# Optimization experiments

Measured on AMD Instinct MI355X. Metric: run time of the kernel, lower is better.

The kernel has to match this reference:

```python
import jax, jax.numpy as jnp
import numpy as np

MIN_NORM = 1e-7

def _norm(x):
    return jnp.maximum(jnp.sqrt(jnp.sum(x * x, axis=-1, keepdims=True)), MIN_NORM)

def _artanh(x):
    return jnp.arctanh(jnp.clip(x, -1.0 + 1e-6, 1.0 - 1e-6))

def tan_k(x, k):
    sq = jnp.sqrt(-k)
    return jnp.tanh(sq * x) / sq

def artan_k(x, k):
    sq = jnp.sqrt(-k)
    return _artanh(sq * x) / sq

def mobius_add(x, y, k):
    xy = jnp.sum(x * y, axis=-1, keepdims=True)
    x2 = jnp.sum(x * x, axis=-1, keepdims=True)
    y2 = jnp.sum(y * y, axis=-1, keepdims=True)
    num = (1.0 - 2.0 * k * xy - k * y2) * x + (1.0 + k * x2) * y
    den = 1.0 - 2.0 * k * xy + (k * k) * x2 * y2
    return num / jnp.maximum(den, MIN_NORM)

def expmap0(u, k):
    un = _norm(u)
    return tan_k(un, k) * u / un

def logmap0(y, k):
    yn = _norm(y)
    return artan_k(yn, k) * y / yn

def mobius_matvec(M, x, k):
    mx = x @ M.T
    xn = _norm(x)
    mxn = _norm(mx)
    return tan_k(mxn / xn * artan_k(xn, k), k) * mx / mxn

def mobius_pmul(w, x, k):
    wx = w * x
    xn = _norm(x)
    wxn = _norm(wx)
    return tan_k(wxn / xn * artan_k(xn, k), k) * wx / wxn

def setup_inputs() -> dict:
    B, S, D_IN, H = 64, 128, 768, 768
    key = jax.random.key(0)
    ks = jax.random.split(key, 5)
    stdv = 1.0 / np.sqrt(H)
    # inputs scaled small so points lie well inside the Poincare ball
    inputs = jax.random.normal(ks[0], (B, S, D_IN), dtype=jnp.float32) * 1e-3
    timestamps = jax.random.uniform(ks[1], (B, S), dtype=jnp.float32)
    h0 = jnp.zeros((B, H), dtype=jnp.float32)
    c0 = jnp.zeros((B, H), dtype=jnp.float32)
    W_all = jax.random.uniform(ks[2], (H, 4 * H), minval=-stdv, maxval=stdv, dtype=jnp.float32)
    U_all = jax.random.uniform(ks[3], (4 * H, D_IN), minval=-stdv, maxval=stdv, dtype=jnp.float32)
    W_d = jax.random.uniform(ks[4], (H, H), minval=-stdv, maxval=stdv, dtype=jnp.float32)
    c = jnp.float32(-1.0)  # Poincare ball curvature
    return {"inputs": inputs, "timestamps": timestamps, "h0": h0, "c0": c0,
            "W_all": W_all, "U_all": U_all, "W_d": W_d, "c": c}

def reference(inputs, timestamps, h0, c0, W_all, U_all, W_d, c):
    k = c
    W_f, W_i, W_o, W_ct = jnp.split(W_all, 4, axis=1)
    U_f, U_i, U_o, U_ct = jnp.split(U_all, 4, axis=0)

    def one_rnn_transform(W, h, U, x):
        return mobius_add(mobius_matvec(W, h, k), mobius_matvec(U, x, k), k)

    def step(carry, xs):
        h, cc = carry
        x, t = xs  # x: (B, D_in), t: (B,)
        c_s1 = expmap0(jnp.tanh(logmap0(mobius_matvec(W_d, cc, k), k)), k)
        t_exp = jnp.broadcast_to(t[:, None], c_s1.shape)
        c_s2 = mobius_pmul(c_s1, t_exp, k)
        c_l = mobius_add(-c_s1, cc, k)
        c_adj = mobius_add(c_l, c_s2, k)
        f = jax.nn.sigmoid(logmap0(one_rnn_transform(W_f, h, U_f, x), k))
        i = jax.nn.sigmoid(logmap0(one_rnn_transform(W_i, h, U_i, x), k))
        o = jax.nn.sigmoid(logmap0(one_rnn_transform(W_o, h, U_o, x), k))
        c_tmp = jax.nn.sigmoid(logmap0(one_rnn_transform(W_ct, h, U_ct, x), k))
        new_c = mobius_add(mobius_pmul(i, c_tmp, k), mobius_pmul(f, c_adj, k), k)
        new_h = mobius_pmul(o, expmap0(jnp.tanh(new_c), k), k)
        return (new_h, new_c), o

    xs = (inputs.transpose(1, 0, 2), timestamps.T)  # seq-major for scan
    (h_last, c_last), outs = jax.lax.scan(step, (h0, c0), xs)
    outputs = outs.transpose(1, 0, 2)  # (B, S, H)
    return (outputs, h_last, c_last)
```

## Files before the change

kernel.cpp:

```cpp
#include <hip/hip_runtime.h>
#include <hip/hip_bf16.h>
#include <math.h>

#define MINN 1e-7f

#define BB 64
#define SS 128
#define NCOL 3840

typedef float f4 __attribute__((ext_vector_type(4)));
typedef short bf16x8 __attribute__((ext_vector_type(8)));
typedef float f32x4 __attribute__((ext_vector_type(4)));

__device__ __forceinline__ float artanh_c(float x) {
  x = fminf(fmaxf(x, -1.0f + 1e-6f), 1.0f - 1e-6f);
  return atanhf(x);
}
__device__ __forceinline__ float tan_k_(float x, float sq) { return tanhf(sq * x) / sq; }
__device__ __forceinline__ float artan_k_(float x, float sq) { return artanh_c(sq * x) / sq; }

template <int N>
__device__ __forceinline__ void block_reduce_sum(float* v, float* red) {
#pragma unroll
  for (int m = 1; m < 64; m <<= 1) {
#pragma unroll
    for (int i = 0; i < N; ++i) v[i] += __shfl_xor(v[i], m, 64);
  }
  int wid = threadIdx.x >> 6;
  int lane = threadIdx.x & 63;
  if (lane == 0) {
#pragma unroll
    for (int i = 0; i < N; ++i) red[wid * N + i] = v[i];
  }
  __syncthreads();
#pragma unroll
  for (int i = 0; i < N; ++i) v[i] = red[i] + red[N + i] + red[2 * N + i] + red[3 * N + i];
  __syncthreads();
}

__global__ __launch_bounds__(256) void k_build_cw(const float* __restrict__ W_all,
                                                  const float* __restrict__ W_d,
                                                  __hip_bfloat16* __restrict__ CWh,
                                                  __hip_bfloat16* __restrict__ CWl) {
  int col = blockIdx.x;
#pragma unroll
  for (int p = 0; p < 3; ++p) {
    int k = threadIdx.x + 256 * p;
    float v;
    if (col < 768) {
      v = W_d[col * 768 + k];
    } else {
      int jm = col - 768;
      int g = jm / 768;
      int j2 = jm - g * 768;
      v = W_all[j2 * 3072 + g * 768 + k];
    }
    __hip_bfloat16 h = __float2bfloat16(v);
    CWh[(size_t)col * 768 + k] = h;
    CWl[(size_t)col * 768 + k] = __float2bfloat16(v - __bfloat162float(h));
  }
}

__global__ __launch_bounds__(256) void k_init_state(
    const float* __restrict__ h0, const float* __restrict__ c0,
    float* __restrict__ ccR, float* __restrict__ hR,
    __hip_bfloat16* __restrict__ CH, __hip_bfloat16* __restrict__ CL,
    __hip_bfloat16* __restrict__ HH, __hip_bfloat16* __restrict__ HL) {
  int r = blockIdx.x;
#pragma unroll
  for (int p = 0; p < 3; ++p) {
    int j = threadIdx.x + 256 * p;
    float cv = c0[r * 768 + j];
    float hv = h0[r * 768 + j];
    ccR[r * 768 + j] = cv;
    hR[r * 768 + j] = hv;
    __hip_bfloat16 ch = __float2bfloat16(cv);
    CH[r * 768 + j] = ch;
    CL[r * 768 + j] = __float2bfloat16(cv - __bfloat162float(ch));
    __hip_bfloat16 hh = __float2bfloat16(hv);
    HH[r * 768 + j] = hh;
    HL[r * 768 + j] = __float2bfloat16(hv - __bfloat162float(hh));
  }
}

__global__ __launch_bounds__(256) void k_xnorm(const float* __restrict__ X,
                                               float* __restrict__ XN) {
  __shared__ float red[4];
  int r = blockIdx.x;
  float s = 0.f;
#pragma unroll
  for (int p = 0; p < 3; ++p) {
    float v = X[(size_t)r * 768 + threadIdx.x + 256 * p];
    s += v * v;
  }
#pragma unroll
  for (int m = 1; m < 64; m <<= 1) s += __shfl_xor(s, m, 64);
  if ((threadIdx.x & 63) == 0) red[threadIdx.x >> 6] = s;
  __syncthreads();
  if (threadIdx.x == 0) XN[r] = fmaxf(sqrtf(red[0] + red[1] + red[2] + red[3]), MINN);
}

__global__ __launch_bounds__(256) void k_split(const float* __restrict__ src,
                                               __hip_bfloat16* __restrict__ hi,
                                               __hip_bfloat16* __restrict__ lo, int n4) {
  int i = blockIdx.x * 256 + threadIdx.x;
  if (i >= n4) return;
  f4 v = *(const f4*)(src + (size_t)i * 4);
#pragma unroll
  for (int j = 0; j < 4; ++j) {
    float x = (j == 0) ? v.x : (j == 1) ? v.y : (j == 2) ? v.z : v.w;
    __hip_bfloat16 h = __float2bfloat16(x);
    float r = x - __bfloat162float(h);
    hi[(size_t)i * 4 + j] = h;
    lo[(size_t)i * 4 + j] = __float2bfloat16(r);
  }
}

__global__ __launch_bounds__(256) void k_gemm_xu_mfma(
    const __hip_bfloat16* __restrict__ Xh, const __hip_bfloat16* __restrict__ Xl,
    const __hip_bfloat16* __restrict__ Uh, __hip_bfloat16* __restrict__ OUT) {
  int tid = threadIdx.x;
  int wave = tid >> 6, lane = tid & 63;
  int r = lane & 15, kg = lane >> 4;
  int i0 = blockIdx.x * 128 + wave * 32;
  int m0 = blockIdx.y * 64;
  const __hip_bfloat16* xh0 = Xh + (size_t)(i0 + r) * 768 + kg * 8;
  const __hip_bfloat16* xh1 = Xh + (size_t)(i0 + 16 + r) * 768 + kg * 8;
  const __hip_bfloat16* xl0 = Xl + (size_t)(i0 + r) * 768 + kg * 8;
  const __hip_bfloat16* xl1 = Xl + (size_t)(i0 + 16 + r) * 768 + kg * 8;
  const __hip_bfloat16* uh = Uh + (size_t)(m0 + r) * 768 + kg * 8;
  f32x4 acc[2][4];
#pragma unroll
  for (int a = 0; a < 2; ++a)
#pragma unroll
    for (int b = 0; b < 4; ++b) acc[a][b] = {0.f, 0.f, 0.f, 0.f};
  for (int k0 = 0; k0 < 768; k0 += 32) {
    bf16x8 ah0 = *(const bf16x8*)(xh0 + k0);
    bf16x8 ah1 = *(const bf16x8*)(xh1 + k0);
    bf16x8 al0 = *(const bf16x8*)(xl0 + k0);
    bf16x8 al1 = *(const bf16x8*)(xl1 + k0);
    bf16x8 bh[4];
#pragma unroll
    for (int p = 0; p < 4; ++p) bh[p] = *(const bf16x8*)(uh + p * 12288 + k0);
#pragma unroll
    for (int p = 0; p < 4; ++p) {
      acc[0][p] = __builtin_amdgcn_mfma_f32_16x16x32_bf16(ah0, bh[p], acc[0][p], 0, 0, 0);
      acc[1][p] = __builtin_amdgcn_mfma_f32_16x16x32_bf16(ah1, bh[p], acc[1][p], 0, 0, 0);
      acc[0][p] = __builtin_amdgcn_mfma_f32_16x16x32_bf16(al0, bh[p], acc[0][p], 0, 0, 0);
      acc[1][p] = __builtin_amdgcn_mfma_f32_16x16x32_bf16(al1, bh[p], acc[1][p], 0, 0, 0);
    }
  }
#pragma unroll
  for (int a = 0; a < 2; ++a)
#pragma unroll
    for (int p = 0; p < 4; ++p)
#pragma unroll
      for (int jj = 0; jj < 4; ++jj)
        OUT[(size_t)(i0 + a * 16 + kg * 4 + jj) * 3072 + m0 + p * 16 + r] =
            __float2bfloat16(acc[a][p][jj]);
}

__global__ __launch_bounds__(256) void k_step_gemm_mfma(
    const __hip_bfloat16* __restrict__ CWh, const __hip_bfloat16* __restrict__ CWl,
    const __hip_bfloat16* __restrict__ CH, const __hip_bfloat16* __restrict__ CL,
    const __hip_bfloat16* __restrict__ HH, const __hip_bfloat16* __restrict__ HL,
    float* __restrict__ GOUT2) {
  int cg = blockIdx.x;
  int kh = blockIdx.y;
  int wave = threadIdx.x >> 6, lane = threadIdx.x & 63;
  int r = lane & 15, kg = lane >> 4;
  int i0 = wave * 16;
  int m0 = cg * 64;
  int kb = kh * 384;
  const __hip_bfloat16* sh = (cg < 12 ? CH : HH) + (size_t)(i0 + r) * 768 + kb + kg * 8;
  const __hip_bfloat16* sl = (cg < 12 ? CL : HL) + (size_t)(i0 + r) * 768 + kb + kg * 8;
  const __hip_bfloat16* wh = CWh + (size_t)(m0 + r) * 768 + kb + kg * 8;
  const __hip_bfloat16* wl = CWl + (size_t)(m0 + r) * 768 + kb + kg * 8;
  f32x4 acc[4];
#pragma unroll
  for (int p = 0; p < 4; ++p) acc[p] = {0.f, 0.f, 0.f, 0.f};
#pragma unroll 4
  for (int k0 = 0; k0 < 384; k0 += 32) {
    bf16x8 ah = *(const bf16x8*)(sh + k0);
    bf16x8 al = *(const bf16x8*)(sl + k0);
#pragma unroll
    for (int p = 0; p < 4; ++p) {
      bf16x8 bh = *(const bf16x8*)(wh + p * 12288 + k0);
      bf16x8 bl = *(const bf16x8*)(wl + p * 12288 + k0);
      acc[p] = __builtin_amdgcn_mfma_f32_16x16x32_bf16(ah, bh, acc[p], 0, 0, 0);
      acc[p] = __builtin_amdgcn_mfma_f32_16x16x32_bf16(al, bh, acc[p], 0, 0, 0);
      acc[p] = __builtin_amdgcn_mfma_f32_16x16x32_bf16(ah, bl, acc[p], 0, 0, 0);
    }
  }
  float* gout = GOUT2 + (size_t)kh * (BB * NCOL);
#pragma unroll
  for (int p = 0; p < 4; ++p)
#pragma unroll
    for (int jj = 0; jj < 4; ++jj)
      gout[(size_t)(i0 + kg * 4 + jj) * NCOL + m0 + p * 16 + r] = acc[p][jj];
}

__global__ __launch_bounds__(256) void k_step_pw(
    const float* __restrict__ GOUT2, const __hip_bfloat16* __restrict__ UG,
    const float* __restrict__ XN, const float* __restrict__ TS,
    const float* __restrict__ kptr, float* __restrict__ ccR, float* __restrict__ hR,
    __hip_bfloat16* __restrict__ CH, __hip_bfloat16* __restrict__ CL,
    __hip_bfloat16* __restrict__ HH, __hip_bfloat16* __restrict__ HL,
    float* __restrict__ out, int t) {
  __shared__ float red[64];
  int r = blockIdx.x;
  int tid = threadIdx.x;
  float kk = kptr[0];
  float sq = sqrtf(-kk);
  const float* grow0 = GOUT2 + (size_t)r * NCOL;
  const float* grow1 = GOUT2 + (size_t)BB * NCOL + (size_t)r * NCOL;
  int i = r * SS + t;
  const __hip_bfloat16* urow = UG + (size_t)i * 3072;

  float cc[3], h[3], mv[3], gh[4][3], mx[4][3];
#pragma unroll
  for (int p = 0; p < 3; ++p) {
    int j = tid + 256 * p;
    cc[p] = ccR[r * 768 + j];
    h[p] = hR[r * 768 + j];
    mv[p] = grow0[j] + grow1[j];
#pragma unroll
    for (int g = 0; g < 4; ++g) {
      gh[g][p] = grow0[768 + g * 768 + j] + grow1[768 + g * 768 + j];
      mx[g][p] = __bfloat162float(urow[g * 768 + j]);
    }
  }

  float sv[15];
#pragma unroll
  for (int q = 0; q < 15; ++q) sv[q] = 0.f;
#pragma unroll
  for (int p = 0; p < 3; ++p) {
    sv[0] += cc[p] * cc[p];
    sv[1] += h[p] * h[p];
    sv[2] += mv[p] * mv[p];
#pragma unroll
    for (int g = 0; g < 4; ++g) {
      sv[3 + g] += gh[g][p] * gh[g][p];
      sv[7 + g] += gh[g][p] * mx[g][p];
      sv[11 + g] += mx[g][p] * mx[g][p];
    }
  }
  block_reduce_sum<15>(sv, red);
  float c2 = sv[0], h2 = sv[1], mvn2 = sv[2];
  float xn_c = fmaxf(sqrtf(c2), MINN);
  float xn_h = fmaxf(sqrtf(h2), MINN);
  float mxn_d = fmaxf(sqrtf(mvn2), MINN);

  float r_d = (mxn_d / xn_c) * artan_k_(xn_c, sq);
  float twd = tan_k_(r_d, sq);
  float wdsc = twd / mxn_d;
  float yn_d = fmaxf(fabsf(twd), MINN);
  float lsc = (artan_k_(yn_d, sq) / yn_d) * wdsc;
  float th[3];
#pragma unroll
  for (int p = 0; p < 3; ++p) th[p] = tanhf(lsc * mv[p]);

  float uxn = XN[i];
  float ak_h = artan_k_(xn_h, sq);
  float ak_u = artan_k_(uxn, sq);
  float cAg[4], cBg[4], pscg[4];
#pragma unroll
  for (int g = 0; g < 4; ++g) {
    float ghn = fmaxf(sqrtf(sv[3 + g]), MINN);
    float tg = tan_k_((ghn / xn_h) * ak_h, sq);
    float wsc = tg / ghn;
    float w2 = tg * tg;
    float umxn = fmaxf(sqrtf(sv[11 + g]), MINN);
    float us = tan_k_((umxn / uxn) * ak_u, sq) / umxn;
    float u2 = us * us * sv[11 + g];
    float xy = wsc * us * sv[7 + g];
    float den = fmaxf(1.f - 2.f * kk * xy + kk * kk * w2 * u2, MINN);
    float a = (1.f - 2.f * kk * xy - kk * u2) / den;
    float b = (1.f + kk * w2) / den;
    float y2s = fmaxf(a * a * w2 + 2.f * a * b * xy + b * b * u2, 0.f);
    float yn = fmaxf(sqrtf(y2s), MINN);
    pscg[g] = artan_k_(yn, sq) / yn;
    cAg[g] = a * wsc;
    cBg[g] = b * us;
  }
  float gate[4][3];
#pragma unroll
  for (int g = 0; g < 4; ++g)
#pragma unroll
    for (int p = 0; p < 3; ++p)
      gate[g][p] = 1.f / (1.f + expf(-pscg[g] * (cAg[g] * gh[g][p] + cBg[g] * mx[g][p])));

  float s2v[2] = {0.f, 0.f};
#pragma unroll
  for (int p = 0; p < 3; ++p) {
    s2v[0] += th[p] * th[p];
    s2v[1] += th[p] * cc[p];
  }
  block_reduce_sum<2>(s2v, red);
  float un = fmaxf(sqrtf(s2v[0]), MINN);
  float esc = tan_k_(un, sq) / un;
  float cs1[3];
#pragma unroll
  for (int p = 0; p < 3; ++p) cs1[p] = esc * th[p];
  float d1 = esc * s2v[1];
  float s1sq = esc * esc * s2v[0];

  float tv = TS[r * SS + t];
  float xnt = fmaxf(sqrtf(768.f * tv * tv), MINN);
  float wxn_t = fmaxf(fabsf(tv) * sqrtf(s1sq), MINN);
  float s2s = tan_k_((wxn_t / xnt) * artan_k_(xnt, sq), sq) / wxn_t * tv;
  float s2sq = s2s * s2s * s1sq;

  float den_l = fmaxf(1.f + 2.f * kk * d1 + kk * kk * s1sq * c2, MINN);
  float al = (1.f + 2.f * kk * d1 - kk * c2) / den_l;
  float bl = (1.f + kk * s1sq) / den_l;
  float pcl = -al, qcl = bl;

  float xy2 = s2s * (pcl * s1sq + qcl * d1);
  float x2b = fmaxf(pcl * pcl * s1sq + 2.f * pcl * qcl * d1 + qcl * qcl * c2, 0.f);
  float y2b = s2sq;
  float den2 = fmaxf(1.f - 2.f * kk * xy2 + kk * kk * x2b * y2b, MINN);
  float a2 = (1.f - 2.f * kk * xy2 - kk * y2b) / den2;
  float b2 = (1.f + kk * x2b) / den2;
  float g1c = a2 * pcl + b2 * s2s;
  float g2c = a2 * qcl;
  float cadj[3];
#pragma unroll
  for (int p = 0; p < 3; ++p) cadj[p] = g1c * cs1[p] + g2c * cc[p];
  float adjsq = fmaxf(g1c * g1c * s1sq + 2.f * g1c * g2c * d1 + g2c * g2c * c2, 0.f);

  float wxi[3], wxf[3];
#pragma unroll
  for (int p = 0; p < 3; ++p) {
    wxi[p] = gate[1][p] * gate[3][p];
    wxf[p] = gate[0][p] * cadj[p];
  }
  float s3v[4] = {0.f, 0.f, 0.f, 0.f};
#pragma unroll
  for (int p = 0; p < 3; ++p) {
    s3v[0] += gate[3][p] * gate[3][p];
    s3v[1] += wxi[p] * wxi[p];
    s3v[2] += wxf[p] * wxf[p];
    s3v[3] += wxi[p] * wxf[p];
  }
  block_reduce_sum<4>(s3v, red);
  float xnct = fmaxf(sqrtf(s3v[0]), MINN);
  float wxni = fmaxf(sqrtf(s3v[1]), MINN);
  float psi = tan_k_((wxni / xnct) * artan_k_(xnct, sq), sq) / wxni;
  float pi2 = psi * psi * s3v[1];
  float xnadj = fmaxf(sqrtf(adjsq), MINN);
  float wxnf = fmaxf(sqrtf(s3v[2]), MINN);
  float psf = tan_k_((wxnf / xnadj) * artan_k_(xnadj, sq), sq) / wxnf;
  float pf2 = psf * psf * s3v[2];
  float xyp = psi * psf * s3v[3];
  float den3 = fmaxf(1.f - 2.f * kk * xyp + kk * kk * pi2 * pf2, MINN);
  float a3 = (1.f - 2.f * kk * xyp - kk * pf2) / den3;
  float b3 = (1.f + kk * pi2) / den3;
  float nc[3], tc[3];
#pragma unroll
  for (int p = 0; p < 3; ++p) {
    nc[p] = a3 * psi * wxi[p] + b3 * psf * wxf[p];
    tc[p] = tanhf(nc[p]);
  }
  float s4v[2] = {0.f, 0.f};
#pragma unroll
  for (int p = 0; p < 3; ++p) {
    s4v[0] += tc[p] * tc[p];
    float gt = gate[2][p] * tc[p];
    s4v[1] += gt * gt;
  }
  block_reduce_sum<2>(s4v, red);
  float unh = fmaxf(sqrtf(s4v[0]), MINN);
  float ehs = tan_k_(unh, sq) / unh;
  float Esq = ehs * ehs * s4v[0];
  float En = fmaxf(sqrtf(Esq), MINN);
  float wxno = fmaxf(ehs * sqrtf(s4v[1]), MINN);
  float pso = tan_k_((wxno / En) * artan_k_(En, sq), sq) / wxno;

  size_t BSHc = (size_t)BB * SS * 768;
#pragma unroll
  for (int p = 0; p < 3; ++p) {
    int j = tid + 256 * p;
    out[((size_t)r * SS + t) * 768 + j] = gate[2][p];
    float ncv = nc[p];
    float nhv = pso * (gate[2][p] * (ehs * tc[p]));
    ccR[r * 768 + j] = ncv;
    hR[r * 768 + j] = nhv;
    __hip_bfloat16 chh = __float2bfloat16(ncv);
    CH[r * 768 + j] = chh;
    CL[r * 768 + j] = __float2bfloat16(ncv - __bfloat162float(chh));
    __hip_bfloat16 hhh = __float2bfloat16(nhv);
    HH[r * 768 + j] = hhh;
    HL[r * 768 + j] = __float2bfloat16(nhv - __bfloat162float(hhh));
    if (t == SS - 1) {
      out[BSHc + (size_t)r * 768 + j] = nhv;
      out[BSHc + (size_t)BB * 768 + (size_t)r * 768 + j] = ncv;
    }
  }
}

extern "C" void kernel_launch(void* const* d_in, const int* in_sizes, int n_in,
                              void* d_out, int out_size, void* d_ws, size_t ws_size,
                              hipStream_t stream) {
  const float* inputs = (const float*)d_in[0];
  const float* ts = (const float*)d_in[1];
  const float* h0 = (const float*)d_in[2];
  const float* c0 = (const float*)d_in[3];
  const float* W_all = (const float*)d_in[4];
  const float* U_all = (const float*)d_in[5];
  const float* W_d = (const float*)d_in[6];
  const float* kptr = (const float*)d_in[7];
  float* ws = (float*)d_ws;
  float* out = (float*)d_out;

  size_t oCWH = 0;
  size_t oCWL = oCWH + 1474560;
  size_t oCCR = oCWL + 1474560;
  size_t oHR = oCCR + 49152;
  size_t oCH = oHR + 49152;
  size_t oCL = oCH + 24576;
  size_t oHH = oCL + 24576;
  size_t oHL = oHH + 24576;
  size_t oGOUT = oHL + 24576;
  size_t oXN = oGOUT + 2 * (size_t)BB * NCOL;
  size_t oUG = oXN + 8192;
  size_t oXH = oUG + 12582912;
  size_t oXL = oXH + 3145728;
  size_t oUH = oXL + 3145728;
  size_t oUL = oUH + 1179648;

  __hip_bfloat16* cwh = (__hip_bfloat16*)(ws + oCWH);
  __hip_bfloat16* cwl = (__hip_bfloat16*)(ws + oCWL);
  float* ccr = ws + oCCR;
  float* hr = ws + oHR;
  __hip_bfloat16* ch = (__hip_bfloat16*)(ws + oCH);
  __hip_bfloat16* cl = (__hip_bfloat16*)(ws + oCL);
  __hip_bfloat16* hh = (__hip_bfloat16*)(ws + oHH);
  __hip_bfloat16* hl = (__hip_bfloat16*)(ws + oHL);
  float* gout = ws + oGOUT;
  float* xn = ws + oXN;
  __hip_bfloat16* ug = (__hip_bfloat16*)(ws + oUG);
  __hip_bfloat16* xhh = (__hip_bfloat16*)(ws + oXH);
  __hip_bfloat16* xll = (__hip_bfloat16*)(ws + oXL);
  __hip_bfloat16* uhh = (__hip_bfloat16*)(ws + oUH);
  __hip_bfloat16* ull = (__hip_bfloat16*)(ws + oUL);

  k_build_cw<<<NCOL, 256, 0, stream>>>(W_all, W_d, cwh, cwl);
  k_init_state<<<BB, 256, 0, stream>>>(h0, c0, ccr, hr, ch, cl, hh, hl);
  k_split<<<(6291456 / 4 + 255) / 256, 256, 0, stream>>>(inputs, xhh, xll, 6291456 / 4);
  k_split<<<(2359296 / 4 + 255) / 256, 256, 0, stream>>>(U_all, uhh, ull, 2359296 / 4);
  k_gemm_xu_mfma<<<dim3(64, 48), 256, 0, stream>>>(xhh, xll, uhh, ug);
  k_xnorm<<<BB * SS, 256, 0, stream>>>(inputs, xn);

  for (int t = 0; t < SS; ++t) {
    k_step_gemm_mfma<<<dim3(60, 2), 256, 0, stream>>>(cwh, cwl, ch, cl, hh, hl, gout);
    k_step_pw<<<BB, 256, 0, stream>>>(gout, ug, xn, ts, kptr, ccr, hr, ch, cl, hh, hl,
                                      out, t);
  }
}
```

Before: 4.119 ms.

## Fuse per-step GEMM and pointwise kernels using a flag-based grid barrier

Merges the recurrent step GEMM and the pointwise gate update into one kernel launched with 120 workgroups. Each workgroup computes its GEMM tile, writes partial sums with volatile stores, and publishes a per-step generation flag. The first 64 workgroups spin on all flags before running the pointwise phase. This removes one kernel launch and its launch gap per timestep, but depends on all workgroups being co-resident and on relaxed atomics without explicit fences for memory ordering.

```diff
diff --git a/kernel.cpp b/kernel.cpp
--- a/kernel.cpp
+++ b/kernel.cpp
@@ -7,6 +7,7 @@
 #define BB 64
 #define SS 128
 #define NCOL 3840
+#define NWG_STEP 120
 
 typedef float f4 __attribute__((ext_vector_type(4)));
 typedef short bf16x8 __attribute__((ext_vector_type(8)));
@@ -160,56 +161,72 @@
             __float2bfloat16(acc[a][p][jj]);
 }
 
-__global__ __launch_bounds__(256) void k_step_gemm_mfma(
+__global__ __launch_bounds__(256) void k_step(
     const __hip_bfloat16* __restrict__ CWh, const __hip_bfloat16* __restrict__ CWl,
     const __hip_bfloat16* __restrict__ CH, const __hip_bfloat16* __restrict__ CL,
     const __hip_bfloat16* __restrict__ HH, const __hip_bfloat16* __restrict__ HL,
-    float* __restrict__ GOUT2) {
-  int cg = blockIdx.x;
-  int kh = blockIdx.y;
-  int wave = threadIdx.x >> 6, lane = threadIdx.x & 63;
-  int r = lane & 15, kg = lane >> 4;
-  int i0 = wave * 16;
-  int m0 = cg * 64;
-  int kb = kh * 384;
-  const __hip_bfloat16* sh = (cg < 12 ? CH : HH) + (size_t)(i0 + r) * 768 + kb + kg * 8;
-  const __hip_bfloat16* sl = (cg < 12 ? CL : HL) + (size_t)(i0 + r) * 768 + kb + kg * 8;
-  const __hip_bfloat16* wh = CWh + (size_t)(m0 + r) * 768 + kb + kg * 8;
-  const __hip_bfloat16* wl = CWl + (size_t)(m0 + r) * 768 + kb + kg * 8;
-  f32x4 acc[4];
-#pragma unroll
-  for (int p = 0; p < 4; ++p) acc[p] = {0.f, 0.f, 0.f, 0.f};
-#pragma unroll 4
-  for (int k0 = 0; k0 < 384; k0 += 32) {
-    bf16x8 ah = *(const bf16x8*)(sh + k0);
-    bf16x8 al = *(const bf16x8*)(sl + k0);
-#pragma unroll
-    for (int p = 0; p < 4; ++p) {
-      bf16x8 bh = *(const bf16x8*)(wh + p * 12288 + k0);
-      bf16x8 bl = *(const bf16x8*)(wl + p * 12288 + k0);
-      acc[p] = __builtin_amdgcn_mfma_f32_16x16x32_bf16(ah, bh, acc[p], 0, 0, 0);
-      acc[p] = __builtin_amdgcn_mfma_f32_16x16x32_bf16(al, bh, acc[p], 0, 0, 0);
-      acc[p] = __builtin_amdgcn_mfma_f32_16x16x32_bf16(ah, bl, acc[p], 0, 0, 0);
-    }
-  }
-  float* gout = GOUT2 + (size_t)kh * (BB * NCOL);
-#pragma unroll
-  for (int p = 0; p < 4; ++p)
-#pragma unroll
-    for (int jj = 0; jj < 4; ++jj)
-      gout[(size_t)(i0 + kg * 4 + jj) * NCOL + m0 + p * 16 + r] = acc[p][jj];
-}
-
-__global__ __launch_bounds__(256) void k_step_pw(
-    const float* __restrict__ GOUT2, const __hip_bfloat16* __restrict__ UG,
-    const float* __restrict__ XN, const float* __restrict__ TS,
-    const float* __restrict__ kptr, float* __restrict__ ccR, float* __restrict__ hR,
-    __hip_bfloat16* __restrict__ CH, __hip_bfloat16* __restrict__ CL,
-    __hip_bfloat16* __restrict__ HH, __hip_bfloat16* __restrict__ HL,
+    float* __restrict__ GOUT2, unsigned int* __restrict__ flags,
+    const __hip_bfloat16* __restrict__ UG, const float* __restrict__ XN,
+    const float* __restrict__ TS, const float* __restrict__ kptr,
+    float* __restrict__ ccR, float* __restrict__ hR,
+    __hip_bfloat16* __restrict__ CHo, __hip_bfloat16* __restrict__ CLo,
+    __hip_bfloat16* __restrict__ HHo, __hip_bfloat16* __restrict__ HLo,
     float* __restrict__ out, int t) {
   __shared__ float red[64];
-  int r = blockIdx.x;
+  int wg = blockIdx.x;
   int tid = threadIdx.x;
+  unsigned int gen = (unsigned int)(t + 1);
+
+  {
+    int cg = wg % 60;
+    int kh = wg / 60;
+    int wave = tid >> 6, lane = tid & 63;
+    int r = lane & 15, kg = lane >> 4;
+    int i0 = wave * 16;
+    int m0 = cg * 64;
+    int kb = kh * 384;
+    const __hip_bfloat16* sh = (cg < 12 ? CH : HH) + (size_t)(i0 + r) * 768 + kb + kg * 8;
+    const __hip_bfloat16* sl = (cg < 12 ? CL : HL) + (size_t)(i0 + r) * 768 + kb + kg * 8;
+    const __hip_bfloat16* wh = CWh + (size_t)(m0 + r) * 768 + kb + kg * 8;
+    const __hip_bfloat16* wl = CWl + (size_t)(m0 + r) * 768 + kb + kg * 8;
+    f32x4 acc[4];
+#pragma unroll
+    for (int p = 0; p < 4; ++p) acc[p] = {0.f, 0.f, 0.f, 0.f};
+#pragma unroll 4
+    for (int k0 = 0; k0 < 384; k0 += 32) {
+      bf16x8 ah = *(const bf16x8*)(sh + k0);
+      bf16x8 al = *(const bf16x8*)(sl + k0);
+#pragma unroll
+      for (int p = 0; p < 4; ++p) {
+        bf16x8 bh = *(const bf16x8*)(wh + p * 12288 + k0);
+        bf16x8 bl = *(const bf16x8*)(wl + p * 12288 + k0);
+        acc[p] = __builtin_amdgcn_mfma_f32_16x16x32_bf16(ah, bh, acc[p], 0, 0, 0);
+        acc[p] = __builtin_amdgcn_mfma_f32_16x16x32_bf16(al, bh, acc[p], 0, 0, 0);
+        acc[p] = __builtin_amdgcn_mfma_f32_16x16x32_bf16(ah, bl, acc[p], 0, 0, 0);
+      }
+    }
+    float* gout = GOUT2 + (size_t)kh * (BB * NCOL);
+#pragma unroll
+    for (int p = 0; p < 4; ++p)
+#pragma unroll
+      for (int jj = 0; jj < 4; ++jj)
+        *(volatile float*)&gout[(size_t)(i0 + kg * 4 + jj) * NCOL + m0 + p * 16 + r] =
+            acc[p][jj];
+  }
+  __syncthreads();
+  if (tid == 0)
+    __hip_atomic_store(&flags[wg], gen, __ATOMIC_RELAXED, __HIP_MEMORY_SCOPE_AGENT);
+  if (wg >= BB) return;
+
+  if (tid < NWG_STEP) {
+    while (__hip_atomic_load(&flags[tid], __ATOMIC_RELAXED, __HIP_MEMORY_SCOPE_AGENT) <
+           gen) {
+      __builtin_amdgcn_s_sleep(4);
+    }
+  }
+  __syncthreads();
+
+  int r = wg;
   float kk = kptr[0];
   float sq = sqrtf(-kk);
   const float* grow0 = GOUT2 + (size_t)r * NCOL;
@@ -223,10 +240,11 @@
     int j = tid + 256 * p;
     cc[p] = ccR[r * 768 + j];
     h[p] = hR[r * 768 + j];
-    mv[p] = grow0[j] + grow1[j];
+    mv[p] = *(volatile const float*)&grow0[j] + *(volatile const float*)&grow1[j];
 #pragma unroll
     for (int g = 0; g < 4; ++g) {
-      gh[g][p] = grow0[768 + g * 768 + j] + grow1[768 + g * 768 + j];
+      gh[g][p] = *(volatile const float*)&grow0[768 + g * 768 + j] +
+                 *(volatile const float*)&grow1[768 + g * 768 + j];
       mx[g][p] = __bfloat162float(urow[g * 768 + j]);
     }
   }
@@ -388,11 +406,11 @@
     ccR[r * 768 + j] = ncv;
     hR[r * 768 + j] = nhv;
     __hip_bfloat16 chh = __float2bfloat16(ncv);
-    CH[r * 768 + j] = chh;
-    CL[r * 768 + j] = __float2bfloat16(ncv - __bfloat162float(chh));
+    CHo[r * 768 + j] = chh;
+    CLo[r * 768 + j] = __float2bfloat16(ncv - __bfloat162float(chh));
     __hip_bfloat16 hhh = __float2bfloat16(nhv);
-    HH[r * 768 + j] = hhh;
-    HL[r * 768 + j] = __float2bfloat16(nhv - __bfloat162float(hhh));
+    HHo[r * 768 + j] = hhh;
+    HLo[r * 768 + j] = __float2bfloat16(nhv - __bfloat162float(hhh));
     if (t == SS - 1) {
       out[BSHc + (size_t)r * 768 + j] = nhv;
       out[BSHc + (size_t)BB * 768 + (size_t)r * 768 + j] = ncv;
@@ -414,7 +432,8 @@
   float* ws = (float*)d_ws;
   float* out = (float*)d_out;
 
-  size_t oCWH = 0;
+  size_t oFLG = 0;
+  size_t oCWH = 128;
   size_t oCWL = oCWH + 1474560;
   size_t oCCR = oCWL + 1474560;
   size_t oHR = oCCR + 49152;
@@ -430,6 +449,7 @@
   size_t oUH = oXL + 3145728;
   size_t oUL = oUH + 1179648;
 
+  unsigned int* flags = (unsigned int*)(ws + oFLG);
   __hip_bfloat16* cwh = (__hip_bfloat16*)(ws + oCWH);
   __hip_bfloat16* cwl = (__hip_bfloat16*)(ws + oCWL);
   float* ccr = ws + oCCR;
@@ -446,6 +466,7 @@
   __hip_bfloat16* uhh = (__hip_bfloat16*)(ws + oUH);
   __hip_bfloat16* ull = (__hip_bfloat16*)(ws + oUL);
 
+  hipMemsetAsync(flags, 0, 512, stream);
   k_build_cw<<<NCOL, 256, 0, stream>>>(W_all, W_d, cwh, cwl);
   k_init_state<<<BB, 256, 0, stream>>>(h0, c0, ccr, hr, ch, cl, hh, hl);
   k_split<<<(6291456 / 4 + 255) / 256, 256, 0, stream>>>(inputs, xhh, xll, 6291456 / 4);
@@ -454,8 +475,7 @@
   k_xnorm<<<BB * SS, 256, 0, stream>>>(inputs, xn);
 
   for (int t = 0; t < SS; ++t) {
-    k_step_gemm_mfma<<<dim3(60, 2), 256, 0, stream>>>(cwh, cwl, ch, cl, hh, hl, gout);
-    k_step_pw<<<BB, 256, 0, stream>>>(gout, ug, xn, ts, kptr, ccr, hr, ch, cl, hh, hl,
-                                      out, t);
-  }
-}
+    k_step<<<NWG_STEP, 256, 0, stream>>>(cwh, cwl, ch, cl, hh, hl, gout, flags, ug, xn,
+                                         ts, kptr, ccr, hr, ch, cl, hh, hl, out, t);
+  }
+}
```

Measured after the change: 5.958 ms. 44.6% more time.

## Fuse recurrent scan into one persistent per-row kernel with fp16 dot2

Applied to the files above, without the earlier changes.

Replaces the per-timestep MFMA GEMM and pointwise kernel launches with a single persistent kernel where each block owns one batch row for all timesteps. State is kept in shared memory, and the recurrent matvecs use packed fp16 fdot2 against a pre-packed weight layout, with a hi/lo split for the cell state. This removes 256 launches and the global round-trips of the state. In exchange, every block re-streams the full weight matrix each step, only 64 workgroups run, and hidden-state precision drops to fp16.

```diff
diff --git a/kernel.cpp b/kernel.cpp
--- a/kernel.cpp
+++ b/kernel.cpp
@@ -3,7 +3,6 @@
 #include <math.h>
 
 #define MINN 1e-7f
-
 #define BB 64
 #define SS 128
 #define NCOL 3840
@@ -11,6 +10,7 @@
 typedef float f4 __attribute__((ext_vector_type(4)));
 typedef short bf16x8 __attribute__((ext_vector_type(8)));
 typedef float f32x4 __attribute__((ext_vector_type(4)));
+typedef _Float16 h2 __attribute__((ext_vector_type(2)));
 
 __device__ __forceinline__ float artanh_c(float x) {
   x = fminf(fmaxf(x, -1.0f + 1e-6f), 1.0f - 1e-6f);
@@ -19,67 +19,74 @@
 __device__ __forceinline__ float tan_k_(float x, float sq) { return tanhf(sq * x) / sq; }
 __device__ __forceinline__ float artan_k_(float x, float sq) { return artanh_c(sq * x) / sq; }
 
+__device__ __forceinline__ float fdot2u(unsigned wa, unsigned wb, float c) {
+  union U { unsigned u; h2 v; };
+  U A, B;
+  A.u = wa;
+  B.u = wb;
+#if __has_builtin(__builtin_amdgcn_fdot2)
+  return __builtin_amdgcn_fdot2(A.v, B.v, c, false);
+#else
+  return c + (float)A.v.x * (float)B.v.x + (float)A.v.y * (float)B.v.y;
+#endif
+}
+
+__device__ __forceinline__ unsigned pk16(float a, float b) {
+  union U { h2 v; unsigned u; } X;
+  X.v.x = (_Float16)a;
+  X.v.y = (_Float16)b;
+  return X.u;
+}
+__device__ __forceinline__ void unpk(unsigned u, float& x, float& y) {
+  union U { unsigned u; h2 v; } X;
+  X.u = u;
+  x = (float)X.v.x;
+  y = (float)X.v.y;
+}
+
 template <int N>
-__device__ __forceinline__ void block_reduce_sum(float* v, float* red) {
-#pragma unroll
-  for (int m = 1; m < 64; m <<= 1) {
+__device__ __forceinline__ void redu12(float* v, float* red) {
+#pragma unroll
+  for (int m = 1; m < 64; m <<= 1)
 #pragma unroll
     for (int i = 0; i < N; ++i) v[i] += __shfl_xor(v[i], m, 64);
-  }
-  int wid = threadIdx.x >> 6;
-  int lane = threadIdx.x & 63;
-  if (lane == 0) {
+  int wid = threadIdx.x >> 6, lane = threadIdx.x & 63;
+  if (lane == 0)
 #pragma unroll
     for (int i = 0; i < N; ++i) red[wid * N + i] = v[i];
-  }
   __syncthreads();
 #pragma unroll
-  for (int i = 0; i < N; ++i) v[i] = red[i] + red[N + i] + red[2 * N + i] + red[3 * N + i];
+  for (int i = 0; i < N; ++i) {
+    float s = 0.f;
+#pragma unroll
+    for (int w = 0; w < 12; ++w) s += red[w * N + i];
+    v[i] = s;
+  }
   __syncthreads();
 }
 
-__global__ __launch_bounds__(256) void k_build_cw(const float* __restrict__ W_all,
+__global__ __launch_bounds__(256) void k_build_w4(const float* __restrict__ W_all,
                                                   const float* __restrict__ W_d,
-                                                  __hip_bfloat16* __restrict__ CWh,
-                                                  __hip_bfloat16* __restrict__ CWl) {
-  int col = blockIdx.x;
-#pragma unroll
-  for (int p = 0; p < 3; ++p) {
-    int k = threadIdx.x + 256 * p;
-    float v;
-    if (col < 768) {
-      v = W_d[col * 768 + k];
-    } else {
-      int jm = col - 768;
-      int g = jm / 768;
-      int j2 = jm - g * 768;
-      v = W_all[j2 * 3072 + g * 768 + k];
-    }
-    __hip_bfloat16 h = __float2bfloat16(v);
-    CWh[(size_t)col * 768 + k] = h;
-    CWl[(size_t)col * 768 + k] = __float2bfloat16(v - __bfloat162float(h));
-  }
-}
-
-__global__ __launch_bounds__(256) void k_init_state(
-    const float* __restrict__ h0, const float* __restrict__ c0,
-    float* __restrict__ ccR, float* __restrict__ hR,
-    __hip_bfloat16* __restrict__ CH, __hip_bfloat16* __restrict__ CL,
-    __hip_bfloat16* __restrict__ HH, __hip_bfloat16* __restrict__ HL) {
-  int r = blockIdx.x;
-#pragma unroll
-  for (int p = 0; p < 3; ++p) {
-    int j = threadIdx.x + 256 * p;
-    float cv = c0[r * 768 + j];
-    float hv = h0[r * 768 + j];
-    ccR[r * 768 + j] = cv;
-    hR[r * 768 + j] = hv;
-    __hip_bfloat16 ch = __float2bfloat16(cv);
-    CH[r * 768 + j] = ch;
-    CL[r * 768 + j] = __float2bfloat16(cv - __bfloat162float(ch));
-    __hip_bfloat16 hh = __float2bfloat16(hv);
-    HH[r * 768 + j] = hh;
-    HL[r * 768 + j] = __float2bfloat16(hv - __bfloat162float(hh));
+                                                  uint2* __restrict__ W4) {
+  int k4 = blockIdx.x;
+  for (int col = threadIdx.x; col < NCOL; col += 256) {
+    float v[4];
+#pragma unroll
+    for (int q = 0; q < 4; ++q) {
+      int k = 4 * k4 + q;
+      if (col < 768) {
+        v[q] = W_d[col * 768 + k];
+      } else {
+        int jm = col - 768;
+        int g = jm / 768;
+        int m = jm - g * 768;
+        v[q] = W_all[m * 3072 + g * 768 + k];
+      }
+    }
+    uint2 w;
+    w.x = pk16(v[0], v[1]);
+    w.y = pk16(v[2], v[3]);
+    W4[(size_t)k4 * NCOL + col] = w;
   }
 }
 
@@ -160,243 +167,198 @@
             __float2bfloat16(acc[a][p][jj]);
 }
 
-__global__ __launch_bounds__(256) void k_step_gemm_mfma(
-    const __hip_bfloat16* __restrict__ CWh, const __hip_bfloat16* __restrict__ CWl,
-    const __hip_bfloat16* __restrict__ CH, const __hip_bfloat16* __restrict__ CL,
-    const __hip_bfloat16* __restrict__ HH, const __hip_bfloat16* __restrict__ HL,
-    float* __restrict__ GOUT2) {
-  int cg = blockIdx.x;
-  int kh = blockIdx.y;
-  int wave = threadIdx.x >> 6, lane = threadIdx.x & 63;
-  int r = lane & 15, kg = lane >> 4;
-  int i0 = wave * 16;
-  int m0 = cg * 64;
-  int kb = kh * 384;
-  const __hip_bfloat16* sh = (cg < 12 ? CH : HH) + (size_t)(i0 + r) * 768 + kb + kg * 8;
-  const __hip_bfloat16* sl = (cg < 12 ? CL : HL) + (size_t)(i0 + r) * 768 + kb + kg * 8;
-  const __hip_bfloat16* wh = CWh + (size_t)(m0 + r) * 768 + kb + kg * 8;
-  const __hip_bfloat16* wl = CWl + (size_t)(m0 + r) * 768 + kb + kg * 8;
-  f32x4 acc[4];
-#pragma unroll
-  for (int p = 0; p < 4; ++p) acc[p] = {0.f, 0.f, 0.f, 0.f};
-#pragma unroll 4
-  for (int k0 = 0; k0 < 384; k0 += 32) {
-    bf16x8 ah = *(const bf16x8*)(sh + k0);
-    bf16x8 al = *(const bf16x8*)(sl + k0);
-#pragma unroll
-    for (int p = 0; p < 4; ++p) {
-      bf16x8 bh = *(const bf16x8*)(wh + p * 12288 + k0);
-      bf16x8 bl = *(const bf16x8*)(wl + p * 12288 + k0);
-      acc[p] = __builtin_amdgcn_mfma_f32_16x16x32_bf16(ah, bh, acc[p], 0, 0, 0);
-      acc[p] = __builtin_amdgcn_mfma_f32_16x16x32_bf16(al, bh, acc[p], 0, 0, 0);
-      acc[p] = __builtin_amdgcn_mfma_f32_16x16x32_bf16(ah, bl, acc[p], 0, 0, 0);
-    }
-  }
-  float* gout = GOUT2 + (size_t)kh * (BB * NCOL);
-#pragma unroll
-  for (int p = 0; p < 4; ++p)
-#pragma unroll
-    for (int jj = 0; jj < 4; ++jj)
-      gout[(size_t)(i0 + kg * 4 + jj) * NCOL + m0 + p * 16 + r] = acc[p][jj];
-}
-
-__global__ __launch_bounds__(256) void k_step_pw(
-    const float* __restrict__ GOUT2, const __hip_bfloat16* __restrict__ UG,
+__global__ __launch_bounds__(768, 1) void k_scan_rows(
+    const uint2* __restrict__ W4, const __hip_bfloat16* __restrict__ UG,
     const float* __restrict__ XN, const float* __restrict__ TS,
-    const float* __restrict__ kptr, float* __restrict__ ccR, float* __restrict__ hR,
-    __hip_bfloat16* __restrict__ CH, __hip_bfloat16* __restrict__ CL,
-    __hip_bfloat16* __restrict__ HH, __hip_bfloat16* __restrict__ HL,
-    float* __restrict__ out, int t) {
-  __shared__ float red[64];
+    const float* __restrict__ kptr, const float* __restrict__ h0,
+    const float* __restrict__ c0, float* __restrict__ out) {
+  __shared__ float sc32[768], sh32[768];
+  __shared__ unsigned scHi[384], scLo[384], shHi[384];
+  __shared__ float red[12 * 15];
   int r = blockIdx.x;
   int tid = threadIdx.x;
   float kk = kptr[0];
   float sq = sqrtf(-kk);
-  const float* grow0 = GOUT2 + (size_t)r * NCOL;
-  const float* grow1 = GOUT2 + (size_t)BB * NCOL + (size_t)r * NCOL;
-  int i = r * SS + t;
-  const __hip_bfloat16* urow = UG + (size_t)i * 3072;
-
-  float cc[3], h[3], mv[3], gh[4][3], mx[4][3];
-#pragma unroll
-  for (int p = 0; p < 3; ++p) {
-    int j = tid + 256 * p;
-    cc[p] = ccR[r * 768 + j];
-    h[p] = hR[r * 768 + j];
-    mv[p] = grow0[j] + grow1[j];
+
+  sc32[tid] = c0[r * 768 + tid];
+  sh32[tid] = h0[r * 768 + tid];
+  __syncthreads();
+  if (tid < 384) {
+    float a = sc32[2 * tid], b = sc32[2 * tid + 1];
+    unsigned hi = pk16(a, b);
+    float hx, hy;
+    unpk(hi, hx, hy);
+    scHi[tid] = hi;
+    scLo[tid] = pk16(a - hx, b - hy);
+    shHi[tid] = pk16(sh32[2 * tid], sh32[2 * tid + 1]);
+  }
+  __syncthreads();
+
+  size_t BSHc = (size_t)BB * SS * 768;
+
+  for (int t = 0; t < SS; ++t) {
+    int i = r * SS + t;
+    const __hip_bfloat16* urow = UG + (size_t)i * 3072;
+    float mx[4];
+#pragma unroll
+    for (int g = 0; g < 4; ++g) mx[g] = __bfloat162float(urow[g * 768 + tid]);
+    float tv = TS[i];
+    float uxn = XN[i];
+
+    float a0 = 0.f, a0l = 0.f, a1 = 0.f, a2v = 0.f, a3v = 0.f, a4v = 0.f;
+    {
+      const uint2* wp = W4 + tid;
+      const uint2* cH = (const uint2*)scHi;
+      const uint2* cL = (const uint2*)scLo;
+      const uint2* hH = (const uint2*)shHi;
+#pragma unroll 4
+      for (int k4 = 0; k4 < 192; ++k4) {
+        uint2 c2 = cH[k4], l2 = cL[k4], hh = hH[k4];
+        uint2 w0 = wp[(size_t)k4 * NCOL];
+        uint2 w1 = wp[(size_t)k4 * NCOL + 768];
+        uint2 w2 = wp[(size_t)k4 * NCOL + 1536];
+        uint2 w3 = wp[(size_t)k4 * NCOL + 2304];
+        uint2 w4v = wp[(size_t)k4 * NCOL + 3072];
+        a0 = fdot2u(w0.x, c2.x, a0);
+        a0 = fdot2u(w0.y, c2.y, a0);
+        a0l = fdot2u(w0.x, l2.x, a0l);
+        a0l = fdot2u(w0.y, l2.y, a0l);
+        a1 = fdot2u(w1.x, hh.x, a1);
+        a1 = fdot2u(w1.y, hh.y, a1);
+        a2v = fdot2u(w2.x, hh.x, a2v);
+        a2v = fdot2u(w2.y, hh.y, a2v);
+        a3v = fdot2u(w3.x, hh.x, a3v);
+        a3v = fdot2u(w3.y, hh.y, a3v);
+        a4v = fdot2u(w4v.x, hh.x, a4v);
+        a4v = fdot2u(w4v.y, hh.y, a4v);
+      }
+    }
+    float mv = a0 + a0l;
+    float gh[4] = {a1, a2v, a3v, a4v};
+    float cc = sc32[tid];
+    float h = sh32[tid];
+
+    float sv[15];
+    sv[0] = cc * cc;
+    sv[1] = h * h;
+    sv[2] = mv * mv;
 #pragma unroll
     for (int g = 0; g < 4; ++g) {
-      gh[g][p] = grow0[768 + g * 768 + j] + grow1[768 + g * 768 + j];
-      mx[g][p] = __bfloat162float(urow[g * 768 + j]);
-    }
-  }
-
-  float sv[15];
-#pragma unroll
-  for (int q = 0; q < 15; ++q) sv[q] = 0.f;
-#pragma unroll
-  for (int p = 0; p < 3; ++p) {
-    sv[0] += cc[p] * cc[p];
-    sv[1] += h[p] * h[p];
-    sv[2] += mv[p] * mv[p];
+      sv[3 + g] = gh[g] * gh[g];
+      sv[7 + g] = gh[g] * mx[g];
+      sv[11 + g] = mx[g] * mx[g];
+    }
+    redu12<15>(sv, red);
+    float c2s = sv[0], h2s = sv[1], mvn2 = sv[2];
+    float xn_c = fmaxf(sqrtf(c2s), MINN);
+    float xn_h = fmaxf(sqrtf(h2s), MINN);
+    float mxn_d = fmaxf(sqrtf(mvn2), MINN);
+
+    float r_d = (mxn_d / xn_c) * artan_k_(xn_c, sq);
+    float twd = tan_k_(r_d, sq);
+    float wdsc = twd / mxn_d;
+    float yn_d = fmaxf(fabsf(twd), MINN);
+    float lsc = (artan_k_(yn_d, sq) / yn_d) * wdsc;
+    float th = tanhf(lsc * mv);
+
+    float ak_h = artan_k_(xn_h, sq);
+    float ak_u = artan_k_(uxn, sq);
+    float gate[4];
 #pragma unroll
     for (int g = 0; g < 4; ++g) {
-      sv[3 + g] += gh[g][p] * gh[g][p];
-      sv[7 + g] += gh[g][p] * mx[g][p];
-      sv[11 + g] += mx[g][p] * mx[g][p];
-    }
-  }
-  block_reduce_sum<15>(sv, red);
-  float c2 = sv[0], h2 = sv[1], mvn2 = sv[2];
-  float xn_c = fmaxf(sqrtf(c2), MINN);
-  float xn_h = fmaxf(sqrtf(h2), MINN);
-  float mxn_d = fmaxf(sqrtf(mvn2), MINN);
-
-  float r_d = (mxn_d / xn_c) * artan_k_(xn_c, sq);
-  float twd = tan_k_(r_d, sq);
-  float wdsc = twd / mxn_d;
-  float yn_d = fmaxf(fabsf(twd), MINN);
-  float lsc = (artan_k_(yn_d, sq) / yn_d) * wdsc;
-  float th[3];
-#pragma unroll
-  for (int p = 0; p < 3; ++p) th[p] = tanhf(lsc * mv[p]);
-
-  float uxn = XN[i];
-  float ak_h = artan_k_(xn_h, sq);
-  float ak_u = artan_k_(uxn, sq);
-  float cAg[4], cBg[4], pscg[4];
-#pragma unroll
-  for (int g = 0; g < 4; ++g) {
-    float ghn = fmaxf(sqrtf(sv[3 + g]), MINN);
-    float tg = tan_k_((ghn / xn_h) * ak_h, sq);
-    float wsc = tg / ghn;
-    float w2 = tg * tg;
-    float umxn = fmaxf(sqrtf(sv[11 + g]), MINN);
-    float us = tan_k_((umxn / uxn) * ak_u, sq) / umxn;
-    float u2 = us * us * sv[11 + g];
-    float xy = wsc * us * sv[7 + g];
-    float den = fmaxf(1.f - 2.f * kk * xy + kk * kk * w2 * u2, MINN);
-    float a = (1.f - 2.f * kk * xy - kk * u2) / den;
-    float b = (1.f + kk * w2) / den;
-    float y2s = fmaxf(a * a * w2 + 2.f * a * b * xy + b * b * u2, 0.f);
-    float yn = fmaxf(sqrtf(y2s), MINN);
-    pscg[g] = artan_k_(yn, sq) / yn;
-    cAg[g] = a * wsc;
-    cBg[g] = b * us;
-  }
-  float gate[4][3];
-#pragma unroll
-  for (int g = 0; g < 4; ++g)
-#pragma unroll
-    for (int p = 0; p < 3; ++p)
-      gate[g][p] = 1.f / (1.f + expf(-pscg[g] * (cAg[g] * gh[g][p] + cBg[g] * mx[g][p])));
-
-  float s2v[2] = {0.f, 0.f};
-#pragma unroll
-  for (int p = 0; p < 3; ++p) {
-    s2v[0] += th[p] * th[p];
-    s2v[1] += th[p] * cc[p];
-  }
-  block_reduce_sum<2>(s2v, red);
-  float un = fmaxf(sqrtf(s2v[0]), MINN);
-  float esc = tan_k_(un, sq) / un;
-  float cs1[3];
-#pragma unroll
-  for (int p = 0; p < 3; ++p) cs1[p] = esc * th[p];
-  float d1 = esc * s2v[1];
-  float s1sq = esc * esc * s2v[0];
-
-  float tv = TS[r * SS + t];
-  float xnt = fmaxf(sqrtf(768.f * tv * tv), MINN);
-  float wxn_t = fmaxf(fabsf(tv) * sqrtf(s1sq), MINN);
-  float s2s = tan_k_((wxn_t / xnt) * artan_k_(xnt, sq), sq) / wxn_t * tv;
-  float s2sq = s2s * s2s * s1sq;
-
-  float den_l = fmaxf(1.f + 2.f * kk * d1 + kk * kk * s1sq * c2, MINN);
-  float al = (1.f + 2.f * kk * d1 - kk * c2) / den_l;
-  float bl = (1.f + kk * s1sq) / den_l;
-  float pcl = -al, qcl = bl;
-
-  float xy2 = s2s * (pcl * s1sq + qcl * d1);
-  float x2b = fmaxf(pcl * pcl * s1sq + 2.f * pcl * qcl * d1 + qcl * qcl * c2, 0.f);
-  float y2b = s2sq;
-  float den2 = fmaxf(1.f - 2.f * kk * xy2 + kk * kk * x2b * y2b, MINN);
-  float a2 = (1.f - 2.f * kk * xy2 - kk * y2b) / den2;
-  float b2 = (1.f + kk * x2b) / den2;
-  float g1c = a2 * pcl + b2 * s2s;
-  float g2c = a2 * qcl;
-  float cadj[3];
-#pragma unroll
-  for (int p = 0; p < 3; ++p) cadj[p] = g1c * cs1[p] + g2c * cc[p];
-  float adjsq = fmaxf(g1c * g1c * s1sq + 2.f * g1c * g2c * d1 + g2c * g2c * c2, 0.f);
-
-  float wxi[3], wxf[3];
-#pragma unroll
-  for (int p = 0; p < 3; ++p) {
-    wxi[p] = gate[1][p] * gate[3][p];
-    wxf[p] = gate[0][p] * cadj[p];
-  }
-  float s3v[4] = {0.f, 0.f, 0.f, 0.f};
-#pragma unroll
-  for (int p = 0; p < 3; ++p) {
-    s3v[0] += gate[3][p] * gate[3][p];
-    s3v[1] += wxi[p] * wxi[p];
-    s3v[2] += wxf[p] * wxf[p];
-    s3v[3] += wxi[p] * wxf[p];
-  }
-  block_reduce_sum<4>(s3v, red);
-  float xnct = fmaxf(sqrtf(s3v[0]), MINN);
-  float wxni = fmaxf(sqrtf(s3v[1]), MINN);
-  float psi = tan_k_((wxni / xnct) * artan_k_(xnct, sq), sq) / wxni;
-  float pi2 = psi * psi * s3v[1];
-  float xnadj = fmaxf(sqrtf(adjsq), MINN);
-  float wxnf = fmaxf(sqrtf(s3v[2]), MINN);
-  float psf = tan_k_((wxnf / xnadj) * artan_k_(xnadj, sq), sq) / wxnf;
-  float pf2 = psf * psf * s3v[2];
-  float xyp = psi * psf * s3v[3];
-  float den3 = fmaxf(1.f - 2.f * kk * xyp + kk * kk * pi2 * pf2, MINN);
-  float a3 = (1.f - 2.f * kk * xyp - kk * pf2) / den3;
-  float b3 = (1.f + kk * pi2) / den3;
-  float nc[3], tc[3];
-#pragma unroll
-  for (int p = 0; p < 3; ++p) {
-    nc[p] = a3 * psi * wxi[p] + b3 * psf * wxf[p];
-    tc[p] = tanhf(nc[p]);
-  }
-  float s4v[2] = {0.f, 0.f};
-#pragma unroll
-  for (int p = 0; p < 3; ++p) {
-    s4v[0] += tc[p] * tc[p];
-    float gt = gate[2][p] * tc[p];
-    s4v[1] += gt * gt;
-  }
-  block_reduce_sum<2>(s4v, red);
-  float unh = fmaxf(sqrtf(s4v[0]), MINN);
-  float ehs = tan_k_(unh, sq) / unh;
-  float Esq = ehs * ehs * s4v[0];
-  float En = fmaxf(sqrtf(Esq), MINN);
-  float wxno = fmaxf(ehs * sqrtf(s4v[1]), MINN);
-  float pso = tan_k_((wxno / En) * artan_k_(En, sq), sq) / wxno;
-
-  size_t BSHc = (size_t)BB * SS * 768;
-#pragma unroll
-  for (int p = 0; p < 3; ++p) {
-    int j = tid + 256 * p;
-    out[((size_t)r * SS + t) * 768 + j] = gate[2][p];
-    float ncv = nc[p];
-    float nhv = pso * (gate[2][p] * (ehs * tc[p]));
-    ccR[r * 768 + j] = ncv;
-    hR[r * 768 + j] = nhv;
-    __hip_bfloat16 chh = __float2bfloat16(ncv);
-    CH[r * 768 + j] = chh;
-    CL[r * 768 + j] = __float2bfloat16(ncv - __bfloat162float(chh));
-    __hip_bfloat16 hhh = __float2bfloat16(nhv);
-    HH[r * 768 + j] = hhh;
-    HL[r * 768 + j] = __float2bfloat16(nhv - __bfloat162float(hhh));
+      float ghn = fmaxf(sqrtf(sv[3 + g]), MINN);
+      float tg = tan_k_((ghn / xn_h) * ak_h, sq);
+      float wsc = tg / ghn;
+      float w2s = tg * tg;
+      float umxn = fmaxf(sqrtf(sv[11 + g]), MINN);
+      float us = tan_k_((umxn / uxn) * ak_u, sq) / umxn;
+      float u2 = us * us * sv[11 + g];
+      float xy = wsc * us * sv[7 + g];
+      float den = fmaxf(1.f - 2.f * kk * xy + kk * kk * w2s * u2, MINN);
+      float aa = (1.f - 2.f * kk * xy - kk * u2) / den;
+      float bb = (1.f + kk * w2s) / den;
+      float y2s = fmaxf(aa * aa * w2s + 2.f * aa * bb * xy + bb * bb * u2, 0.f);
+      float yn = fmaxf(sqrtf(y2s), MINN);
+      float psc = artan_k_(yn, sq) / yn;
+      gate[g] = 1.f / (1.f + expf(-psc * (aa * wsc * gh[g] + bb * us * mx[g])));
+    }
+
+    float s2v[2] = {th * th, th * cc};
+    redu12<2>(s2v, red);
+    float un = fmaxf(sqrtf(s2v[0]), MINN);
+    float esc = tan_k_(un, sq) / un;
+    float cs1 = esc * th;
+    float d1 = esc * s2v[1];
+    float s1sq = esc * esc * s2v[0];
+
+    float xnt = fmaxf(sqrtf(768.f * tv * tv), MINN);
+    float wxn_t = fmaxf(fabsf(tv) * sqrtf(s1sq), MINN);
+    float s2s = tan_k_((wxn_t / xnt) * artan_k_(xnt, sq), sq) / wxn_t * tv;
+    float s2sq = s2s * s2s * s1sq;
+
+    float den_l = fmaxf(1.f + 2.f * kk * d1 + kk * kk * s1sq * c2s, MINN);
+    float al = (1.f + 2.f * kk * d1 - kk * c2s) / den_l;
+    float bl = (1.f + kk * s1sq) / den_l;
+    float pcl = -al, qcl = bl;
+
+    float xy2 = s2s * (pcl * s1sq + qcl * d1);
+    float x2b = fmaxf(pcl * pcl * s1sq + 2.f * pcl * qcl * d1 + qcl * qcl * c2s, 0.f);
+    float y2b = s2sq;
+    float den2 = fmaxf(1.f - 2.f * kk * xy2 + kk * kk * x2b * y2b, MINN);
+    float a2c = (1.f - 2.f * kk * xy2 - kk * y2b) / den2;
+    float b2c = (1.f + kk * x2b) / den2;
+    float g1c = a2c * pcl + b2c * s2s;
+    float g2c = a2c * qcl;
+    float cadj = g1c * cs1 + g2c * cc;
+    float adjsq = fmaxf(g1c * g1c * s1sq + 2.f * g1c * g2c * d1 + g2c * g2c * c2s, 0.f);
+
+    float wxi = gate[1] * gate[3];
+    float wxf = gate[0] * cadj;
+    float s3v[4] = {gate[3] * gate[3], wxi * wxi, wxf * wxf, wxi * wxf};
+    redu12<4>(s3v, red);
+    float xnct = fmaxf(sqrtf(s3v[0]), MINN);
+    float wxni = fmaxf(sqrtf(s3v[1]), MINN);
+    float psi = tan_k_((wxni / xnct) * artan_k_(xnct, sq), sq) / wxni;
+    float pi2 = psi * psi * s3v[1];
+    float xnadj = fmaxf(sqrtf(adjsq), MINN);
+    float wxnf = fmaxf(sqrtf(s3v[2]), MINN);
+    float psf = tan_k_((wxnf / xnadj) * artan_k_(xnadj, sq), sq) / wxnf;
+    float pf2 = psf * psf * s3v[2];
+    float xyp = psi * psf * s3v[3];
+    float den3 = fmaxf(1.f - 2.f * kk * xyp + kk * kk * pi2 * pf2, MINN);
+    float a3c = (1.f - 2.f * kk * xyp - kk * pf2) / den3;
+    float b3c = (1.f + kk * pi2) / den3;
+    float nc = a3c * psi * wxi + b3c * psf * wxf;
+    float tc = tanhf(nc);
+    float gt = gate[2] * tc;
+    float s4v[2] = {tc * tc, gt * gt};
+    redu12<2>(s4v, red);
+    float unh = fmaxf(sqrtf(s4v[0]), MINN);
+    float ehs = tan_k_(unh, sq) / unh;
+    float Esq = ehs * ehs * s4v[0];
+    float En = fmaxf(sqrtf(Esq), MINN);
+    float wxno = fmaxf(ehs * sqrtf(s4v[1]), MINN);
+    float pso = tan_k_((wxno / En) * artan_k_(En, sq), sq) / wxno;
+
+    out[((size_t)r * SS + t) * 768 + tid] = gate[2];
+    float nh = pso * (gate[2] * (ehs * tc));
+    sc32[tid] = nc;
+    sh32[tid] = nh;
     if (t == SS - 1) {
-      out[BSHc + (size_t)r * 768 + j] = nhv;
-      out[BSHc + (size_t)BB * 768 + (size_t)r * 768 + j] = ncv;
-    }
+      out[BSHc + (size_t)r * 768 + tid] = nh;
+      out[BSHc + (size_t)BB * 768 + (size_t)r * 768 + tid] = nc;
+    }
+    __syncthreads();
+    if (t < SS - 1 && tid < 384) {
+      float a = sc32[2 * tid], b = sc32[2 * tid + 1];
+      unsigned hi = pk16(a, b);
+      float hx, hy;
+      unpk(hi, hx, hy);
+      scHi[tid] = hi;
+      scLo[tid] = pk16(a - hx, b - hy);
+      shHi[tid] = pk16(sh32[2 * tid], sh32[2 * tid + 1]);
+    }
+    __syncthreads();
   }
 }
 
@@ -414,31 +376,15 @@
   float* ws = (float*)d_ws;
   float* out = (float*)d_out;
 
-  size_t oCWH = 0;
-  size_t oCWL = oCWH + 1474560;
-  size_t oCCR = oCWL + 1474560;
-  size_t oHR = oCCR + 49152;
-  size_t oCH = oHR + 49152;
-  size_t oCL = oCH + 24576;
-  size_t oHH = oCL + 24576;
-  size_t oHL = oHH + 24576;
-  size_t oGOUT = oHL + 24576;
-  size_t oXN = oGOUT + 2 * (size_t)BB * NCOL;
+  size_t oW4 = 0;
+  size_t oXN = oW4 + 1474560;
   size_t oUG = oXN + 8192;
   size_t oXH = oUG + 12582912;
   size_t oXL = oXH + 3145728;
   size_t oUH = oXL + 3145728;
   size_t oUL = oUH + 1179648;
 
-  __hip_bfloat16* cwh = (__hip_bfloat16*)(ws + oCWH);
-  __hip_bfloat16* cwl = (__hip_bfloat16*)(ws + oCWL);
-  float* ccr = ws + oCCR;
-  float* hr = ws + oHR;
-  __hip_bfloat16* ch = (__hip_bfloat16*)(ws + oCH);
-  __hip_bfloat16* cl = (__hip_bfloat16*)(ws + oCL);
-  __hip_bfloat16* hh = (__hip_bfloat16*)(ws + oHH);
-  __hip_bfloat16* hl = (__hip_bfloat16*)(ws + oHL);
-  float* gout = ws + oGOUT;
+  uint2* w4 = (uint2*)(ws + oW4);
   float* xn = ws + oXN;
   __hip_bfloat16* ug = (__hip_bfloat16*)(ws + oUG);
   __hip_bfloat16* xhh = (__hip_bfloat16*)(ws + oXH);
@@ -446,16 +392,10 @@
   __hip_bfloat16* uhh = (__hip_bfloat16*)(ws + oUH);
   __hip_bfloat16* ull = (__hip_bfloat16*)(ws + oUL);
 
-  k_build_cw<<<NCOL, 256, 0, stream>>>(W_all, W_d, cwh, cwl);
-  k_init_state<<<BB, 256, 0, stream>>>(h0, c0, ccr, hr, ch, cl, hh, hl);
+  k_build_w4<<<192, 256, 0, stream>>>(W_all, W_d, w4);
   k_split<<<(6291456 / 4 + 255) / 256, 256, 0, stream>>>(inputs, xhh, xll, 6291456 / 4);
   k_split<<<(2359296 / 4 + 255) / 256, 256, 0, stream>>>(U_all, uhh, ull, 2359296 / 4);
   k_gemm_xu_mfma<<<dim3(64, 48), 256, 0, stream>>>(xhh, xll, uhh, ug);
   k_xnorm<<<BB * SS, 256, 0, stream>>>(inputs, xn);
-
-  for (int t = 0; t < SS; ++t) {
-    k_step_gemm_mfma<<<dim3(60, 2), 256, 0, stream>>>(cwh, cwl, ch, cl, hh, hl, gout);
-    k_step_pw<<<BB, 256, 0, stream>>>(gout, ug, xn, ts, kptr, ccr, hr, ch, cl, hh, hl,
-                                      out, t);
-  }
-}
+  k_scan_rows<<<BB, 768, 0, stream>>>(w4, ug, xn, ts, kptr, h0, c0, out);
+}
```

New measurement: 14.53 ms. 3.53x slower.
